# Optimization experiments

Measured on AMD Instinct MI355X. Metric: run time of the kernel, lower is better.

Reference implementation:

```python
import jax, jax.numpy as jnp
import numpy as np

B = 128
N_ATOMS = 4096
NB, NA, NT = 4095, 4094, 4093
MAX_LEN = 5 * NT  # 20465, longest packed column (torsions)
EPS = 1e-8


def setup_inputs() -> dict:
    key = jax.random.key(0)
    ks = jax.random.split(key, 24)
    feats = jnp.zeros((B, MAX_LEN, 9), jnp.float32)
    # col 0: atom type ids
    atoms = jax.random.randint(ks[0], (B, N_ATOMS), 0, 6)
    # col 5: coords, flattened (N_ATOMS, 3)
    coords = jax.random.normal(ks[1], (B, N_ATOMS, 3), jnp.float32) * 5.0
    # col 6: bonds (i, j, type)
    bonds = jnp.stack([
        jax.random.randint(ks[2], (B, NB), 0, N_ATOMS),
        jax.random.randint(ks[3], (B, NB), 0, N_ATOMS),
        jax.random.randint(ks[4], (B, NB), 0, 15)], axis=-1)
    # col 7: angles (i, j, k, type)
    angles = jnp.stack([
        jax.random.randint(ks[5], (B, NA), 0, N_ATOMS),
        jax.random.randint(ks[6], (B, NA), 0, N_ATOMS),
        jax.random.randint(ks[7], (B, NA), 0, N_ATOMS),
        jax.random.randint(ks[8], (B, NA), 0, 13)], axis=-1)
    # col 8: torsions (i, j, k, l, type)
    tors = jnp.stack([
        jax.random.randint(ks[9], (B, NT), 0, N_ATOMS),
        jax.random.randint(ks[10], (B, NT), 0, N_ATOMS),
        jax.random.randint(ks[11], (B, NT), 0, N_ATOMS),
        jax.random.randint(ks[12], (B, NT), 0, N_ATOMS),
        jax.random.randint(ks[13], (B, NT), 0, 25)], axis=-1)
    feats = feats.at[:, :N_ATOMS, 0].set(atoms.astype(jnp.float32))
    feats = feats.at[:, :3 * N_ATOMS, 5].set(coords.reshape(B, -1))
    feats = feats.at[:, :3 * NB, 6].set(bonds.reshape(B, -1).astype(jnp.float32))
    feats = feats.at[:, :4 * NA, 7].set(angles.reshape(B, -1).astype(jnp.float32))
    feats = feats.at[:, :5 * NT, 8].set(tors.reshape(B, -1).astype(jnp.float32))
    lengths = jnp.tile(jnp.array(
        [[N_ATOMS, 0, 0, 0, 0, 3 * N_ATOMS, 3 * NB, 4 * NA, 5 * NT]],
        jnp.int32), (B, 1))
    bond_type = jnp.stack([jnp.ones(15), jax.random.uniform(ks[14], (15,), minval=1.0, maxval=2.0)], -1).astype(jnp.float32)
    angle_type = jnp.stack([jnp.ones(13), jax.random.uniform(ks[15], (13,), minval=1.0, maxval=3.0)], -1).astype(jnp.float32)
    tor_type = jnp.stack([jnp.ones(25), jax.random.uniform(ks[16], (25,), minval=0.0, maxval=3.14)], -1).astype(jnp.float32)
    multiplicity = jax.random.randint(ks[17], (25,), 1, 4)
    opt_pars = jax.random.uniform(ks[18], (47,), minval=0.5, maxval=1.5).astype(jnp.float32)
    return {"features": feats, "lengths": lengths, "bond_type": bond_type,
            "angle_type": angle_type, "tor_type": tor_type,
            "multiplicity": multiplicity, "opt_pars": opt_pars}


def _sample_energy(f, bond_type, angle_type, tor_type, multiplicity, opt_pars):
    coords = f[:3 * N_ATOMS, 5].reshape(-1, 3)                      # [N,3]
    bonds = f[:3 * NB, 6].astype(jnp.int32).reshape(-1, 3)          # [NB,3]
    angles = f[:4 * NA, 7].astype(jnp.int32).reshape(-1, 4)         # [NA,4]
    tors = f[:5 * NT, 8].astype(jnp.int32).reshape(-1, 5)           # [NT,5]

    # bonds: harmonic k*(r - r0)^2
    d = coords[bonds[:, 0]] - coords[bonds[:, 1]]
    r = jnp.sqrt(jnp.sum(d * d, -1) + EPS)
    pb = bond_type[bonds[:, 2]]
    e_bond = opt_pars[0] * jnp.sum(pb[:, 0] * (r - pb[:, 1]) ** 2)

    # angles: harmonic k*(theta - theta0)^2
    v1 = coords[angles[:, 0]] - coords[angles[:, 1]]
    v2 = coords[angles[:, 2]] - coords[angles[:, 1]]
    cosang = jnp.sum(v1 * v2, -1) / (
        jnp.sqrt(jnp.sum(v1 * v1, -1) + EPS) * jnp.sqrt(jnp.sum(v2 * v2, -1) + EPS))
    theta = jnp.arccos(jnp.clip(cosang, -1.0 + 1e-6, 1.0 - 1e-6))
    pa = angle_type[angles[:, 3]]
    e_ang = opt_pars[1] * jnp.sum(pa[:, 0] * (theta - pa[:, 1]) ** 2)

    # torsions: periodic k*(1 + cos(n*phi - delta))
    ci, cj, ck, cl = (coords[tors[:, m]] for m in range(4))
    b1, b2, b3 = cj - ci, ck - cj, cl - ck
    n1 = jnp.cross(b1, b2)
    n2 = jnp.cross(b2, b3)
    b2n = b2 / jnp.sqrt(jnp.sum(b2 * b2, -1, keepdims=True) + EPS)
    m1 = jnp.cross(n1, b2n)
    phi = jnp.arctan2(jnp.sum(m1 * n2, -1), jnp.sum(n1 * n2, -1))
    pt = tor_type[tors[:, 4]]
    n_mult = multiplicity[tors[:, 4]].astype(jnp.float32)
    e_tor = opt_pars[2] * jnp.sum(pt[:, 0] * (1.0 + jnp.cos(n_mult * phi - pt[:, 1])))

    return jnp.stack([e_bond, e_ang, e_tor])


def reference(features, lengths, bond_type, angle_type, tor_type, multiplicity, opt_pars):
    # lengths are uniform across batch (constants above); vmap over batch dim
    return jax.vmap(_sample_energy, in_axes=(0, None, None, None, None, None))(
        features, bond_type, angle_type, tor_type, multiplicity, opt_pars)
```

## Files before the change

kernel.cpp:

```cpp
#include <hip/hip_runtime.h>
#include <math.h>

#define BATCH      128
#define N_ATOMS    4096
#define NB         4095
#define NA         4094
#define NT         4093
#define FSTRIDE    184185
#define TOTAL_F4   5893920u
#define EPSV       1e-8f
#define THREADS    1024
#define WAVES      16
#define TILE_F     1080
#define NTILES     171
#define ATILES     103
#define SCR_F4     272

#define WAVE_LDS_FENCE()  do { asm volatile("" ::: "memory"); \
                               __builtin_amdgcn_wave_barrier(); } while (0)

__global__ __launch_bounds__(THREADS, 1) void
local_energy_fused(const float* __restrict__ F,
                   const float* __restrict__ bond_type,
                   const float* __restrict__ angle_type,
                   const float* __restrict__ tor_type,
                   const int*   __restrict__ multiplicity,
                   const float* __restrict__ opt_pars,
                   float*       __restrict__ out)
{
    __shared__ float scx[N_ATOMS];
    __shared__ float scy[N_ATOMS];
    __shared__ float scz[N_ATOMS];
    __shared__ __align__(16) float4 scr[WAVES][SCR_F4];
    __shared__ unsigned short sbB[2080 * 3];
    __shared__ unsigned short sbA[1560 * 4];
    __shared__ unsigned short sbT[1248 * 5];
    __shared__ float sbt[30], sat[26], stt[50], smu[25];
    __shared__ float sred[WAVES * 3];

    const int b   = blockIdx.x;
    const int x   = b & 7;
    const int g   = b >> 3;
    const int s   = (g & 15) * 8 + x;
    const int p   = g >> 4;
    const int tid = threadIdx.x;
    const int w   = tid >> 6;
    const int l   = tid & 63;
    const size_t sbase = (size_t)s * FSTRIDE;
    const int d = (int)(sbase & 3);
    const float4* __restrict__ F4 = (const float4*)F;

    if (tid < 30)                      sbt[tid]       = bond_type[tid];
    else if (tid >= 32 && tid < 58)    sat[tid - 32]  = angle_type[tid - 32];
    else if (tid >= 64 && tid < 114)   stt[tid - 64]  = tor_type[tid - 64];
    else if (tid >= 128 && tid < 153)  smu[tid - 128] = (float)multiplicity[tid - 128];

    float* const swf = (float*)scr[w];

    const int Alo = p ? 51 : 0;
    const int Ahi = p ? 103 : 51;
    const int cnt_b = p ? 2055 : 2040;
    const int cnt_a = p ? 1560 : 1530;
    const int cnt_t = p ? 1248 : 1224;

    {
        const int nq = (d + TILE_F + 3) >> 2;
        float4 cur[5];
        int t = w;
        {
            const size_t q0 = (sbase + (size_t)t * TILE_F) >> 2;
            #pragma unroll
            for (int i = 0; i < 5; ++i) {
                const int k = l + 64 * i;
                cur[i] = (k < nq) ? F4[q0 + k] : make_float4(0.f, 0.f, 0.f, 0.f);
            }
        }
        for (; t < ATILES; t += WAVES) {
            const int tn = t + WAVES;
            float4 nxt[5];
            #pragma unroll
            for (int i = 0; i < 5; ++i) nxt[i] = make_float4(0.f, 0.f, 0.f, 0.f);
            if (tn < ATILES) {
                const size_t q0 = (sbase + (size_t)tn * TILE_F) >> 2;
                #pragma unroll
                for (int i = 0; i < 5; ++i) {
                    const int k = l + 64 * i;
                    if (k < nq) nxt[i] = F4[q0 + k];
                }
            }
            #pragma unroll
            for (int i = 0; i < 4; ++i) scr[w][l + 64 * i] = cur[i];
            if (l < 15) scr[w][l + 256] = cur[4];
            WAVE_LDS_FENCE();

            const int na = (N_ATOMS - 40 * t < 40) ? N_ATOMS - 40 * t : 40;
            if (l < na) {
                const int base = d + 27 * l;
                const int atom = 40 * t + l;
                scx[atom] = swf[base + 5];
                scy[atom] = swf[base + 14];
                scz[atom] = swf[base + 23];
            }
            if (t >= Alo && t < Ahi) {
                const int lt = t - Alo;
                int nb = NB - 40 * t; nb = (nb > 40) ? 40 : nb;
                if (l < nb) {
                    const int sl = (lt * 40 + l) * 3;
                    const int base = d + 27 * l;
                    sbB[sl + 0] = (unsigned short)(int)swf[base + 6];
                    sbB[sl + 1] = (unsigned short)(int)swf[base + 15];
                    sbB[sl + 2] = (unsigned short)(int)swf[base + 24];
                }
                if (l < 30) {
                    const int sl = (lt * 30 + l) * 4;
                    const int base = d + 36 * l;
                    sbA[sl + 0] = (unsigned short)(int)swf[base + 7];
                    sbA[sl + 1] = (unsigned short)(int)swf[base + 16];
                    sbA[sl + 2] = (unsigned short)(int)swf[base + 25];
                    sbA[sl + 3] = (unsigned short)(int)swf[base + 34];
                }
                if (l < 24) {
                    const int sl = (lt * 24 + l) * 5;
                    const int base = d + 45 * l;
                    sbT[sl + 0] = (unsigned short)(int)swf[base + 8];
                    sbT[sl + 1] = (unsigned short)(int)swf[base + 17];
                    sbT[sl + 2] = (unsigned short)(int)swf[base + 26];
                    sbT[sl + 3] = (unsigned short)(int)swf[base + 35];
                    sbT[sl + 4] = (unsigned short)(int)swf[base + 44];
                }
            }
            WAVE_LDS_FENCE();
            #pragma unroll
            for (int i = 0; i < 5; ++i) cur[i] = nxt[i];
        }
    }
    __syncthreads();

    float e_bond = 0.f, e_ang = 0.f, e_tor = 0.f;

    {
        const int tlo = p ? 137 : 103;
        const int thi = p ? 171 : 137;
        float4 cur[5];
        int t = tlo + w;
        {
            const size_t q0 = (sbase + (size_t)t * TILE_F) >> 2;
            const int nf = (FSTRIDE - t * TILE_F < TILE_F) ? FSTRIDE - t * TILE_F : TILE_F;
            const int nq = (d + nf + 3) >> 2;
            #pragma unroll
            for (int i = 0; i < 5; ++i) {
                const int k = l + 64 * i;
                cur[i] = (k < nq && q0 + k < TOTAL_F4) ? F4[q0 + k]
                                                       : make_float4(0.f, 0.f, 0.f, 0.f);
            }
        }
        for (; t < thi; t += WAVES) {
            const int tn = t + WAVES;
            float4 nxt[5];
            #pragma unroll
            for (int i = 0; i < 5; ++i) nxt[i] = make_float4(0.f, 0.f, 0.f, 0.f);
            if (tn < thi) {
                const size_t q0 = (sbase + (size_t)tn * TILE_F) >> 2;
                const int nf = (FSTRIDE - tn * TILE_F < TILE_F) ? FSTRIDE - tn * TILE_F : TILE_F;
                const int nq = (d + nf + 3) >> 2;
                #pragma unroll
                for (int i = 0; i < 5; ++i) {
                    const int k = l + 64 * i;
                    if (k < nq && q0 + k < TOTAL_F4) nxt[i] = F4[q0 + k];
                }
            }
            #pragma unroll
            for (int i = 0; i < 4; ++i) scr[w][l + 64 * i] = cur[i];
            if (l < 15) scr[w][l + 256] = cur[4];
            WAVE_LDS_FENCE();

            int na = NA - 30 * t; na = (na > 30) ? 30 : na;
            if (l < na) {
                const int base = d + 36 * l;
                const int a0 = (int)swf[base + 7];
                const int a1 = (int)swf[base + 16];
                const int a2 = (int)swf[base + 25];
                const int at = (int)swf[base + 34];
                const float v1x = scx[a0] - scx[a1];
                const float v1y = scy[a0] - scy[a1];
                const float v1z = scz[a0] - scz[a1];
                const float v2x = scx[a2] - scx[a1];
                const float v2y = scy[a2] - scy[a1];
                const float v2z = scz[a2] - scz[a1];
                const float d12 = v1x*v2x + v1y*v2y + v1z*v2z;
                const float n1  = sqrtf(v1x*v1x + v1y*v1y + v1z*v1z + EPSV);
                const float n2  = sqrtf(v2x*v2x + v2y*v2y + v2z*v2z + EPSV);
                float cosang = d12 / (n1 * n2);
                cosang = fminf(fmaxf(cosang, -1.0f + 1e-6f), 1.0f - 1e-6f);
                const float t0 = acosf(cosang) - sat[at * 2 + 1];
                e_ang += sat[at * 2 + 0] * t0 * t0;
            }

            int ntr = NT - 24 * t; ntr = (ntr > 24) ? 24 : ntr;
            if (l < ntr) {
                const int base = d + 45 * l;
                const int ai = (int)swf[base + 8];
                const int aj = (int)swf[base + 17];
                const int ak = (int)swf[base + 26];
                const int al = (int)swf[base + 35];
                const int tt = (int)swf[base + 44];
                const float b1x = scx[aj] - scx[ai], b1y = scy[aj] - scy[ai], b1z = scz[aj] - scz[ai];
                const float b2x = scx[ak] - scx[aj], b2y = scy[ak] - scy[aj], b2z = scz[ak] - scz[aj];
                const float b3x = scx[al] - scx[ak], b3y = scy[al] - scy[ak], b3z = scz[al] - scz[ak];
                const float n1x = b1y*b2z - b1z*b2y;
                const float n1y = b1z*b2x - b1x*b2z;
                const float n1z = b1x*b2y - b1y*b2x;
                const float n2x = b2y*b3z - b2z*b3y;
                const float n2y = b2z*b3x - b2x*b3z;
                const float n2z = b2x*b3y - b2y*b3x;
                const float inv = 1.0f / sqrtf(b2x*b2x + b2y*b2y + b2z*b2z + EPSV);
                const float bnx = b2x * inv, bny = b2y * inv, bnz = b2z * inv;
                const float m1x = n1y*bnz - n1z*bny;
                const float m1y = n1z*bnx - n1x*bnz;
                const float m1z = n1x*bny - n1y*bnx;
                const float phi = atan2f(m1x*n2x + m1y*n2y + m1z*n2z,
                                         n1x*n2x + n1y*n2y + n1z*n2z);
                e_tor += stt[tt * 2 + 0] * (1.0f + cosf(smu[tt] * phi - stt[tt * 2 + 1]));
            }

            WAVE_LDS_FENCE();
            #pragma unroll
            for (int i = 0; i < 5; ++i) cur[i] = nxt[i];
        }
    }

    for (int i = tid; i < cnt_b; i += THREADS) {
        const int a0 = sbB[3 * i + 0];
        const int a1 = sbB[3 * i + 1];
        const int bt = sbB[3 * i + 2];
        const float dx = scx[a0] - scx[a1];
        const float dy = scy[a0] - scy[a1];
        const float dz = scz[a0] - scz[a1];
        const float r  = sqrtf(dx*dx + dy*dy + dz*dz + EPSV);
        const float t0 = r - sbt[bt * 2 + 1];
        e_bond += sbt[bt * 2 + 0] * t0 * t0;
    }
    for (int i = tid; i < cnt_a; i += THREADS) {
        const int a0 = sbA[4 * i + 0];
        const int a1 = sbA[4 * i + 1];
        const int a2 = sbA[4 * i + 2];
        const int at = sbA[4 * i + 3];
        const float v1x = scx[a0] - scx[a1];
        const float v1y = scy[a0] - scy[a1];
        const float v1z = scz[a0] - scz[a1];
        const float v2x = scx[a2] - scx[a1];
        const float v2y = scy[a2] - scy[a1];
        const float v2z = scz[a2] - scz[a1];
        const float d12 = v1x*v2x + v1y*v2y + v1z*v2z;
        const float n1  = sqrtf(v1x*v1x + v1y*v1y + v1z*v1z + EPSV);
        const float n2  = sqrtf(v2x*v2x + v2y*v2y + v2z*v2z + EPSV);
        float cosang = d12 / (n1 * n2);
        cosang = fminf(fmaxf(cosang, -1.0f + 1e-6f), 1.0f - 1e-6f);
        const float t0 = acosf(cosang) - sat[at * 2 + 1];
        e_ang += sat[at * 2 + 0] * t0 * t0;
    }
    for (int i = tid; i < cnt_t; i += THREADS) {
        const int ai = sbT[5 * i + 0];
        const int aj = sbT[5 * i + 1];
        const int ak = sbT[5 * i + 2];
        const int al = sbT[5 * i + 3];
        const int tt = sbT[5 * i + 4];
        const float b1x = scx[aj] - scx[ai], b1y = scy[aj] - scy[ai], b1z = scz[aj] - scz[ai];
        const float b2x = scx[ak] - scx[aj], b2y = scy[ak] - scy[aj], b2z = scz[ak] - scz[aj];
        const float b3x = scx[al] - scx[ak], b3y = scy[al] - scy[ak], b3z = scz[al] - scz[ak];
        const float n1x = b1y*b2z - b1z*b2y;
        const float n1y = b1z*b2x - b1x*b2z;
        const float n1z = b1x*b2y - b1y*b2x;
        const float n2x = b2y*b3z - b2z*b3y;
        const float n2y = b2z*b3x - b2x*b3z;
        const float n2z = b2x*b3y - b2y*b3x;
        const float inv = 1.0f / sqrtf(b2x*b2x + b2y*b2y + b2z*b2z + EPSV);
        const float bnx = b2x * inv, bny = b2y * inv, bnz = b2z * inv;
        const float m1x = n1y*bnz - n1z*bny;
        const float m1y = n1z*bnx - n1x*bnz;
        const float m1z = n1x*bny - n1y*bnx;
        const float phi = atan2f(m1x*n2x + m1y*n2y + m1z*n2z,
                                 n1x*n2x + n1y*n2y + n1z*n2z);
        e_tor += stt[tt * 2 + 0] * (1.0f + cosf(smu[tt] * phi - stt[tt * 2 + 1]));
    }

    for (int off = 32; off > 0; off >>= 1) {
        e_bond += __shfl_down(e_bond, off);
        e_ang  += __shfl_down(e_ang,  off);
        e_tor  += __shfl_down(e_tor,  off);
    }
    if (l == 0) {
        sred[w * 3 + 0] = e_bond;
        sred[w * 3 + 1] = e_ang;
        sred[w * 3 + 2] = e_tor;
    }
    __syncthreads();
    if (tid == 0) {
        float eb = 0.f, ea = 0.f, et = 0.f;
        for (int i = 0; i < WAVES; ++i) {
            eb += sred[i * 3 + 0];
            ea += sred[i * 3 + 1];
            et += sred[i * 3 + 2];
        }
        atomicAdd(&out[s * 3 + 0], opt_pars[0] * eb);
        atomicAdd(&out[s * 3 + 1], opt_pars[1] * ea);
        atomicAdd(&out[s * 3 + 2], opt_pars[2] * et);
    }
}

extern "C" void kernel_launch(void* const* d_in, const int* in_sizes, int n_in,
                              void* d_out, int out_size, void* d_ws, size_t ws_size,
                              hipStream_t stream) {
    const float* F            = (const float*)d_in[0];
    const float* bond_type    = (const float*)d_in[2];
    const float* angle_type   = (const float*)d_in[3];
    const float* tor_type     = (const float*)d_in[4];
    const int*   multiplicity = (const int*)  d_in[5];
    const float* opt_pars     = (const float*)d_in[6];
    float* out = (float*)d_out;

    hipMemsetAsync(out, 0, (size_t)out_size * sizeof(float), stream);

    local_energy_fused<<<dim3(BATCH * 2), dim3(THREADS), 0, stream>>>(
        F, bond_type, angle_type, tor_type, multiplicity, opt_pars, out);
}
```

Measured before the change: 159.0 us.

## Split coordinate gathering between paired blocks and exchange via cooperative grid sync

Before this change, each of the two blocks per sample independently read and deinterleaved all atom-coordinate tiles. Now each block reads only its own half of the tiles, writes its half of the coordinates to a workspace buffer, waits on a cooperative grid-wide sync, and reads the other half back into LDS. The aim is to halve redundant global reads in the load phase. In exchange it adds a grid barrier, a global write/read round trip, and a dependence on cooperative launch with every block co-resident.

```diff
diff --git a/kernel.cpp b/kernel.cpp
--- a/kernel.cpp
+++ b/kernel.cpp
@@ -1,5 +1,8 @@
 #include <hip/hip_runtime.h>
+#include <hip/hip_cooperative_groups.h>
 #include <math.h>
+
+namespace cg = cooperative_groups;
 
 #define BATCH      128
 #define N_ATOMS    4096
@@ -13,20 +16,23 @@
 #define WAVES      16
 #define TILE_F     1080
 #define NTILES     171
-#define ATILES     103
 #define SCR_F4     272
+#define GRID       256
+
+#define PLANE      (BATCH * N_ATOMS)
 
 #define WAVE_LDS_FENCE()  do { asm volatile("" ::: "memory"); \
                                __builtin_amdgcn_wave_barrier(); } while (0)
 
 __global__ __launch_bounds__(THREADS, 1) void
-local_energy_fused(const float* __restrict__ F,
-                   const float* __restrict__ bond_type,
-                   const float* __restrict__ angle_type,
-                   const float* __restrict__ tor_type,
-                   const int*   __restrict__ multiplicity,
-                   const float* __restrict__ opt_pars,
-                   float*       __restrict__ out)
+local_energy_coop(const float* __restrict__ F,
+                  const float* __restrict__ bond_type,
+                  const float* __restrict__ angle_type,
+                  const float* __restrict__ tor_type,
+                  const int*   __restrict__ multiplicity,
+                  const float* __restrict__ opt_pars,
+                  float*       __restrict__ ws,
+                  float*       __restrict__ out)
 {
     __shared__ float scx[N_ATOMS];
     __shared__ float scy[N_ATOMS];
@@ -57,16 +63,16 @@
 
     float* const swf = (float*)scr[w];
 
-    const int Alo = p ? 51 : 0;
-    const int Ahi = p ? 103 : 51;
-    const int cnt_b = p ? 2055 : 2040;
-    const int cnt_a = p ? 1560 : 1530;
-    const int cnt_t = p ? 1248 : 1224;
+    const int Alo = p ? 52 : 0;
+    const int Ahi = p ? 103 : 52;
+    const int cnt_b = p ? 2015 : 2080;
+    const int cnt_a = p ? 1530 : 1560;
+    const int cnt_t = p ? 1224 : 1248;
 
     {
         const int nq = (d + TILE_F + 3) >> 2;
         float4 cur[5];
-        int t = w;
+        int t = Alo + w;
         {
             const size_t q0 = (sbase + (size_t)t * TILE_F) >> 2;
             #pragma unroll
@@ -75,12 +81,12 @@
                 cur[i] = (k < nq) ? F4[q0 + k] : make_float4(0.f, 0.f, 0.f, 0.f);
             }
         }
-        for (; t < ATILES; t += WAVES) {
+        for (; t < Ahi; t += WAVES) {
             const int tn = t + WAVES;
             float4 nxt[5];
             #pragma unroll
             for (int i = 0; i < 5; ++i) nxt[i] = make_float4(0.f, 0.f, 0.f, 0.f);
-            if (tn < ATILES) {
+            if (tn < Ahi) {
                 const size_t q0 = (sbase + (size_t)tn * TILE_F) >> 2;
                 #pragma unroll
                 for (int i = 0; i < 5; ++i) {
@@ -93,45 +99,66 @@
             if (l < 15) scr[w][l + 256] = cur[4];
             WAVE_LDS_FENCE();
 
-            const int na = (N_ATOMS - 40 * t < 40) ? N_ATOMS - 40 * t : 40;
-            if (l < na) {
+            const int lt = t - Alo;
+            int nat = N_ATOMS - 40 * t; nat = (nat > 40) ? 40 : nat;
+            if (l < nat) {
                 const int base = d + 27 * l;
                 const int atom = 40 * t + l;
                 scx[atom] = swf[base + 5];
                 scy[atom] = swf[base + 14];
                 scz[atom] = swf[base + 23];
             }
-            if (t >= Alo && t < Ahi) {
-                const int lt = t - Alo;
-                int nb = NB - 40 * t; nb = (nb > 40) ? 40 : nb;
-                if (l < nb) {
-                    const int sl = (lt * 40 + l) * 3;
-                    const int base = d + 27 * l;
-                    sbB[sl + 0] = (unsigned short)(int)swf[base + 6];
-                    sbB[sl + 1] = (unsigned short)(int)swf[base + 15];
-                    sbB[sl + 2] = (unsigned short)(int)swf[base + 24];
-                }
-                if (l < 30) {
-                    const int sl = (lt * 30 + l) * 4;
-                    const int base = d + 36 * l;
-                    sbA[sl + 0] = (unsigned short)(int)swf[base + 7];
-                    sbA[sl + 1] = (unsigned short)(int)swf[base + 16];
-                    sbA[sl + 2] = (unsigned short)(int)swf[base + 25];
-                    sbA[sl + 3] = (unsigned short)(int)swf[base + 34];
-                }
-                if (l < 24) {
-                    const int sl = (lt * 24 + l) * 5;
-                    const int base = d + 45 * l;
-                    sbT[sl + 0] = (unsigned short)(int)swf[base + 8];
-                    sbT[sl + 1] = (unsigned short)(int)swf[base + 17];
-                    sbT[sl + 2] = (unsigned short)(int)swf[base + 26];
-                    sbT[sl + 3] = (unsigned short)(int)swf[base + 35];
-                    sbT[sl + 4] = (unsigned short)(int)swf[base + 44];
-                }
+            int nb = NB - 40 * t; nb = (nb > 40) ? 40 : nb;
+            if (l < nb) {
+                const int sl = (lt * 40 + l) * 3;
+                const int base = d + 27 * l;
+                sbB[sl + 0] = (unsigned short)(int)swf[base + 6];
+                sbB[sl + 1] = (unsigned short)(int)swf[base + 15];
+                sbB[sl + 2] = (unsigned short)(int)swf[base + 24];
+            }
+            if (l < 30) {
+                const int sl = (lt * 30 + l) * 4;
+                const int base = d + 36 * l;
+                sbA[sl + 0] = (unsigned short)(int)swf[base + 7];
+                sbA[sl + 1] = (unsigned short)(int)swf[base + 16];
+                sbA[sl + 2] = (unsigned short)(int)swf[base + 25];
+                sbA[sl + 3] = (unsigned short)(int)swf[base + 34];
+            }
+            if (l < 24) {
+                const int sl = (lt * 24 + l) * 5;
+                const int base = d + 45 * l;
+                sbT[sl + 0] = (unsigned short)(int)swf[base + 8];
+                sbT[sl + 1] = (unsigned short)(int)swf[base + 17];
+                sbT[sl + 2] = (unsigned short)(int)swf[base + 26];
+                sbT[sl + 3] = (unsigned short)(int)swf[base + 35];
+                sbT[sl + 4] = (unsigned short)(int)swf[base + 44];
             }
             WAVE_LDS_FENCE();
             #pragma unroll
             for (int i = 0; i < 5; ++i) cur[i] = nxt[i];
+        }
+    }
+    __syncthreads();
+
+    {
+        float4* __restrict__ wx = (float4*)(ws + 0 * PLANE + (size_t)s * N_ATOMS);
+        float4* __restrict__ wy = (float4*)(ws + 1 * PLANE + (size_t)s * N_ATOMS);
+        float4* __restrict__ wz = (float4*)(ws + 2 * PLANE + (size_t)s * N_ATOMS);
+        const int own_lo4 = p ? 520 : 0;
+        const int own_n4  = p ? 504 : 520;
+        for (int i = tid; i < own_n4; i += THREADS) {
+            wx[own_lo4 + i] = ((float4*)scx)[own_lo4 + i];
+            wy[own_lo4 + i] = ((float4*)scy)[own_lo4 + i];
+            wz[own_lo4 + i] = ((float4*)scz)[own_lo4 + i];
+        }
+        __threadfence();
+        cg::this_grid().sync();
+        const int oth_lo4 = p ? 0 : 520;
+        const int oth_n4  = p ? 520 : 504;
+        for (int i = tid; i < oth_n4; i += THREADS) {
+            ((float4*)scx)[oth_lo4 + i] = wx[oth_lo4 + i];
+            ((float4*)scy)[oth_lo4 + i] = wy[oth_lo4 + i];
+            ((float4*)scz)[oth_lo4 + i] = wz[oth_lo4 + i];
         }
     }
     __syncthreads();
@@ -318,9 +345,13 @@
     const int*   multiplicity = (const int*)  d_in[5];
     const float* opt_pars     = (const float*)d_in[6];
     float* out = (float*)d_out;
+    float* ws  = (float*)d_ws;
 
     hipMemsetAsync(out, 0, (size_t)out_size * sizeof(float), stream);
 
-    local_energy_fused<<<dim3(BATCH * 2), dim3(THREADS), 0, stream>>>(
-        F, bond_type, angle_type, tor_type, multiplicity, opt_pars, out);
+    void* args[] = { (void*)&F, (void*)&bond_type, (void*)&angle_type,
+                     (void*)&tor_type, (void*)&multiplicity, (void*)&opt_pars,
+                     (void*)&ws, (void*)&out };
+    hipLaunchCooperativeKernel((const void*)local_energy_coop,
+                               dim3(GRID), dim3(THREADS), args, 0, stream);
 }
```

Result: slower. 299.7 us (+88.4%).
